# Performance work log

Hardware: AMD Instinct MI355X
Metric: run time of the kernel (lower is better)

Reference implementation:

```python
import math
import jax, jax.numpy as jnp
import numpy as np

N, D = 16384, 1024


def setup_inputs() -> dict:
    key = jax.random.key(0)
    k1, k2 = jax.random.split(key)
    return {
        "image_embeddings_aligned": jax.random.normal(k1, (N, D), dtype=jnp.float32),
        "text_embeddings_aligned": jax.random.normal(k2, (N, D), dtype=jnp.float32),
        "logit_scale": jnp.asarray(math.log(20.0), dtype=jnp.float32),  # stored as log(init)
        "logit_bias": jnp.asarray(-10.0, dtype=jnp.float32),
    }


def _l2_normalize(x, eps=1e-12):
    # matches F.normalize(p=2, dim=-1)
    n = jnp.linalg.norm(x, axis=-1, keepdims=True)
    return x / jnp.maximum(n, eps)


def reference(image_embeddings_aligned, text_embeddings_aligned, logit_scale, logit_bias):
    img = _l2_normalize(image_embeddings_aligned)
    txt = _l2_normalize(text_embeddings_aligned)
    # [N, N] pairwise logits
    logits = jnp.exp(logit_scale) * jnp.einsum("nd,md->nm", img, txt) + logit_bias
    n = logits.shape[0]
    labels = 2.0 * jnp.eye(n, dtype=logits.dtype) - 1.0  # +1 on diagonal, -1 off
    loss_matrix = jax.nn.log_sigmoid(labels * logits)
    siglip_loss = -jnp.mean(loss_matrix)  # total_loss (structure_lambda == 0)
    return siglip_loss
```

## Files before the change

### kernel.cpp

```cpp
#include <hip/hip_runtime.h>

#define NROWS 16384
#define DIM   1024
#define QSCALE 32.0f
#define E8M0S  0x7A7A7A7Au

typedef int    v4i    __attribute__((ext_vector_type(4)));
typedef int    v8i    __attribute__((ext_vector_type(8)));
typedef float  f32x16 __attribute__((ext_vector_type(16)));

__device__ __forceinline__ void glds16(const void* g, void* l) {
    __builtin_amdgcn_global_load_lds(
        (const __attribute__((address_space(1))) void*)g,
        (__attribute__((address_space(3))) void*)l,
        16, 0, 0);
}

__device__ __forceinline__ float fexp2(float x) {
#if __has_builtin(__builtin_amdgcn_exp2f)
    return __builtin_amdgcn_exp2f(x);
#else
    return exp2f(x);
#endif
}
__device__ __forceinline__ float flog2(float x) {
#if __has_builtin(__builtin_amdgcn_logf)
    return __builtin_amdgcn_logf(x);
#else
    return log2f(x);
#endif
}

__device__ __forceinline__ unsigned fp4_nib(float y) {
    unsigned s = (__float_as_uint(y) >> 31) << 3;
    float a = fminf(fabsf(y), 6.0f);
    unsigned c = (unsigned)(a >= 0.25f) + (unsigned)(a >= 0.75f) +
                 (unsigned)(a >= 1.25f) + (unsigned)(a >= 1.75f) +
                 (unsigned)(a >= 2.5f)  + (unsigned)(a >= 3.5f)  +
                 (unsigned)(a >= 5.0f);
    return c | s;
}

__global__ __launch_bounds__(256) void norm_fused(
    const float* __restrict__ img,
    const float* __restrict__ txt,
    unsigned char* __restrict__ imgQ,
    unsigned char* __restrict__ txtQ,
    const float* __restrict__ lscale,
    const float* __restrict__ lbias,
    float* __restrict__ diagPart) {
    const int t    = threadIdx.x;
    const int lane = t & 63;
    const int wave = t >> 6;
    const int gw   = blockIdx.x * 4 + wave;
    const float sc   = __expf(lscale[0]);
    const float bias = lbias[0];

    for (int row = gw; row < NROWS; row += 8192) {
        const float4* pi = (const float4*)(img + (size_t)row * DIM);
        const float4* pt = (const float4*)(txt + (size_t)row * DIM);
        float4 vi[4], vt[4];
        float ssi = 0.0f, sst = 0.0f, dot = 0.0f;
        #pragma unroll
        for (int j = 0; j < 4; ++j) {
            vi[j] = pi[lane + 64 * j];
            vt[j] = pt[lane + 64 * j];
            ssi += vi[j].x*vi[j].x + vi[j].y*vi[j].y + vi[j].z*vi[j].z + vi[j].w*vi[j].w;
            sst += vt[j].x*vt[j].x + vt[j].y*vt[j].y + vt[j].z*vt[j].z + vt[j].w*vt[j].w;
            dot += vi[j].x*vt[j].x + vi[j].y*vt[j].y + vi[j].z*vt[j].z + vi[j].w*vt[j].w;
        }
        #pragma unroll
        for (int off = 1; off < 64; off <<= 1) {
            ssi += __shfl_xor(ssi, off, 64);
            sst += __shfl_xor(sst, off, 64);
            dot += __shfl_xor(dot, off, 64);
        }
        const float ii = 1.0f / fmaxf(sqrtf(ssi), 1e-12f);
        const float it = 1.0f / fmaxf(sqrtf(sst), 1e-12f);
        if (lane == 0) diagPart[row] = -fmaf(sc, dot * ii * it, bias);

        const float qi = ii * QSCALE, qt = it * QSCALE;
        ushort* oi = (ushort*)(imgQ + (size_t)row * 512);
        ushort* ot = (ushort*)(txtQ + (size_t)row * 512);
        #pragma unroll
        for (int j = 0; j < 4; ++j) {
            unsigned p = fp4_nib(vi[j].x * qi)        | (fp4_nib(vi[j].y * qi) << 4) |
                         (fp4_nib(vi[j].z * qi) << 8) | (fp4_nib(vi[j].w * qi) << 12);
            unsigned q = fp4_nib(vt[j].x * qt)        | (fp4_nib(vt[j].y * qt) << 4) |
                         (fp4_nib(vt[j].z * qt) << 8) | (fp4_nib(vt[j].w * qt) << 12);
            oi[lane + 64 * j] = (ushort)p;
            ot[lane + 64 * j] = (ushort)q;
        }
    }
}

__global__ __launch_bounds__(512, 2) void siglip_gemm(
    const unsigned char* __restrict__ A,
    const unsigned char* __restrict__ B,
    const float* __restrict__ lscale,
    const float* __restrict__ lbias,
    float* __restrict__ gemmPart)
{
    __shared__ unsigned char sA[2][256 * 128];
    __shared__ unsigned char sB[2][256 * 128];
    __shared__ float wred[8];

    const int t    = threadIdx.x;
    const int lane = t & 63;
    const int wave = t >> 6;
    const int wr   = wave >> 2;
    const int wc   = wave & 3;
    const int r31  = lane & 31;
    const int h    = lane >> 5;
    const int xr   = (r31 & 7) ^ ((r31 >> 4) & 1);

    const int b    = blockIdx.x;
    const int xcd  = b & 7;
    const int lb   = b >> 3;
    const int bcol = xcd * 8 + (lb & 7);
    const int brow = lb >> 3;

    const size_t aBase = (size_t)brow * 256;
    const size_t bBase = (size_t)bcol * 256;

    const int srow = lane >> 3;
    const int c0   = (lane & 7) ^ srow;
    const int d01  = (c0 & 1) ? -16 : 16;

    const unsigned char* aP = A + (size_t)(aBase + wave * 32 + srow) * 512 + c0 * 16;
    const unsigned char* bP = B + (size_t)(bBase + wave * 32 + srow) * 512 + c0 * 16;

    int rbA[4], rbB[2];
    #pragma unroll
    for (int i = 0; i < 4; ++i) rbA[i] = (wr * 128 + i * 32 + r31) * 128;
    #pragma unroll
    for (int i = 0; i < 2; ++i) rbB[i] = (wc * 64 + i * 32 + r31) * 128;

    f32x16 acc[4][2] = {};

    {
        char* la = ((char*)sA[0]) + wave * 4096;
        char* lb_ = ((char*)sB[0]) + wave * 4096;
        #pragma unroll
        for (int j = 0; j < 4; ++j) {
            const int tog = ((j >> 1) & 1) ? d01 : 0;
            glds16(aP + j * 8 * 512 + tog, la + j * 1024);
            glds16(bP + j * 8 * 512 + tog, lb_ + j * 1024);
        }
    }

    #pragma unroll
    for (int k = 0; k < 4; ++k) {
        const int cur = k & 1;

        if (k < 3) {
            const unsigned char* aN = aP + (k + 1) * 128;
            const unsigned char* bN = bP + (k + 1) * 128;
            char* la = ((char*)sA[cur ^ 1]) + wave * 4096;
            char* lb_ = ((char*)sB[cur ^ 1]) + wave * 4096;
            #pragma unroll
            for (int j = 0; j < 4; ++j) {
                const int tog = ((j >> 1) & 1) ? d01 : 0;
                glds16(aN + j * 8 * 512 + tog, la + j * 1024);
                glds16(bN + j * 8 * 512 + tog, lb_ + j * 1024);
            }
            asm volatile("s_waitcnt vmcnt(8)" ::: "memory");
        } else {
            asm volatile("s_waitcnt vmcnt(0)" ::: "memory");
        }
        __builtin_amdgcn_s_barrier();

        #pragma unroll
        for (int ks = 0; ks < 4; ++ks) {
            const int s = ((ks * 2 + h) ^ xr) * 16;
            v4i av[4], bv[2];
            #pragma unroll
            for (int i = 0; i < 4; ++i)
                av[i] = *(const v4i*)(sA[cur] + rbA[i] + s);
            #pragma unroll
            for (int n = 0; n < 2; ++n)
                bv[n] = *(const v4i*)(sB[cur] + rbB[n] + s);

            __builtin_amdgcn_s_barrier();
            asm volatile("s_waitcnt lgkmcnt(0)" ::: "memory");
            __builtin_amdgcn_sched_barrier(0);
            __builtin_amdgcn_s_setprio(1);
            #pragma unroll
            for (int mi = 0; mi < 4; ++mi) {
                v8i a8 = __builtin_shufflevector(av[mi], av[mi],
                                                 0, 1, 2, 3, -1, -1, -1, -1);
                #pragma unroll
                for (int ni = 0; ni < 2; ++ni) {
                    v8i b8 = __builtin_shufflevector(bv[ni], bv[ni],
                                                     0, 1, 2, 3, -1, -1, -1, -1);
                    acc[mi][ni] = __builtin_amdgcn_mfma_scale_f32_32x32x64_f8f6f4(
                        a8, b8, acc[mi][ni],
                        4, 4,
                        0, (int)E8M0S,
                        0, (int)E8M0S);
                }
            }
            __builtin_amdgcn_s_setprio(0);
            __builtin_amdgcn_s_barrier();
        }
    }

    const float l2e   = 1.44269504088896341f;
    const float scale = __expf(lscale[0]);
    const float aCo   = scale * l2e;
    const float bCo   = lbias[0] * l2e;
    float local = 0.0f;
    #pragma unroll
    for (int mi = 0; mi < 4; ++mi)
        #pragma unroll
        for (int ni = 0; ni < 2; ++ni)
            #pragma unroll
            for (int r = 0; r < 16; r += 4) {
                float e0 = fexp2(fmaf(aCo, acc[mi][ni][r + 0], bCo));
                float e1 = fexp2(fmaf(aCo, acc[mi][ni][r + 1], bCo));
                float e2 = fexp2(fmaf(aCo, acc[mi][ni][r + 2], bCo));
                float e3 = fexp2(fmaf(aCo, acc[mi][ni][r + 3], bCo));
                float p  = ((1.0f + e0) * (1.0f + e1)) *
                           ((1.0f + e2) * (1.0f + e3));
                local += flog2(p);
            }

    #pragma unroll
    for (int off = 32; off > 0; off >>= 1) local += __shfl_down(local, off, 64);
    if (lane == 0) wred[wave] = local;
    __syncthreads();
    if (t == 0) {
        float tot = 0.0f;
        #pragma unroll
        for (int i = 0; i < 8; ++i) tot += wred[i];
        gemmPart[blockIdx.x] = tot * 0.69314718055994531f;
    }
}

__global__ __launch_bounds__(1024) void finalize_kernel(
    const float* __restrict__ parts, float* __restrict__ out) {
    __shared__ float wr[16];
    const int t    = threadIdx.x;
    const int lane = t & 63;
    const int wave = t >> 6;
    const float4* p4 = (const float4*)parts;
    float s = 0.0f;
    for (int i = t; i < 5120; i += 1024) {
        float4 v = p4[i];
        s += v.x + v.y + v.z + v.w;
    }
    #pragma unroll
    for (int off = 32; off > 0; off >>= 1) s += __shfl_down(s, off, 64);
    if (lane == 0) wr[wave] = s;
    __syncthreads();
    if (t == 0) {
        float tot = 0.0f;
        #pragma unroll
        for (int i = 0; i < 16; ++i) tot += wr[i];
        out[0] = tot / 268435456.0f;
    }
}

extern "C" void kernel_launch(void* const* d_in, const int* in_sizes, int n_in,
                              void* d_out, int out_size, void* d_ws, size_t ws_size,
                              hipStream_t stream) {
    const float* img    = (const float*)d_in[0];
    const float* txt    = (const float*)d_in[1];
    const float* lscale = (const float*)d_in[2];
    const float* lbias  = (const float*)d_in[3];
    float* out = (float*)d_out;

    char* ws = (char*)d_ws;
    unsigned char* imgQ = (unsigned char*)ws;
    unsigned char* txtQ = (unsigned char*)(ws + (size_t)NROWS * 512);
    float* parts   = (float*)(ws + (size_t)2 * NROWS * 512);
    float* diagPart = parts;
    float* gemmPart = parts + NROWS;

    norm_fused<<<2048, 256, 0, stream>>>(img, txt, imgQ, txtQ, lscale, lbias, diagPart);
    siglip_gemm<<<dim3((NROWS / 256) * (NROWS / 256)), 512, 0, stream>>>(
        imgQ, txtQ, lscale, lbias, gemmPart);
    finalize_kernel<<<1, 1024, 0, stream>>>(parts, out);
}
```

Measured before the change: 329.8 us.

## Software-pipeline LDS fragment loads and drop per-substep barriers in MFMA loop

Restructures the inner K loop so the LDS fragments for the next sub-step are loaded into a second register set while the current sub-step's MFMAs run, waiting on lgkmcnt(6) instead of draining all LDS reads. The two workgroup barriers per sub-step are removed. Global-to-LDS prefetch now starts after a full vmcnt(0) wait and barrier at the top of each K step rather than a partial wait. This is meant to hide LDS latency and cut synchronization, at the cost of more registers and less overlap of the global prefetch with the wait.

```diff
diff --git a/kernel.cpp b/kernel.cpp
--- a/kernel.cpp
+++ b/kernel.cpp
@@ -153,6 +153,10 @@
     for (int k = 0; k < 4; ++k) {
         const int cur = k & 1;
 
+        asm volatile("s_waitcnt vmcnt(0)" ::: "memory");
+        __builtin_amdgcn_sched_barrier(0);
+        __builtin_amdgcn_s_barrier();
+
         if (k < 3) {
             const unsigned char* aN = aP + (k + 1) * 128;
             const unsigned char* bN = bP + (k + 1) * 128;
@@ -164,44 +168,57 @@
                 glds16(aN + j * 8 * 512 + tog, la + j * 1024);
                 glds16(bN + j * 8 * 512 + tog, lb_ + j * 1024);
             }
-            asm volatile("s_waitcnt vmcnt(8)" ::: "memory");
-        } else {
-            asm volatile("s_waitcnt vmcnt(0)" ::: "memory");
-        }
-        __builtin_amdgcn_s_barrier();
+        }
+
+        v4i pa[2][4], pb[2][2];
+        {
+            const int s0 = (h ^ xr) * 16;
+            #pragma unroll
+            for (int i = 0; i < 4; ++i)
+                pa[0][i] = *(const v4i*)(sA[cur] + rbA[i] + s0);
+            #pragma unroll
+            for (int n = 0; n < 2; ++n)
+                pb[0][n] = *(const v4i*)(sB[cur] + rbB[n] + s0);
+        }
 
         #pragma unroll
         for (int ks = 0; ks < 4; ++ks) {
-            const int s = ((ks * 2 + h) ^ xr) * 16;
-            v4i av[4], bv[2];
+            const int pc = ks & 1, pn = pc ^ 1;
+            if (ks < 3) {
+                const int s1 = (((ks + 1) * 2 + h) ^ xr) * 16;
+                #pragma unroll
+                for (int i = 0; i < 4; ++i)
+                    pa[pn][i] = *(const v4i*)(sA[cur] + rbA[i] + s1);
+                #pragma unroll
+                for (int n = 0; n < 2; ++n)
+                    pb[pn][n] = *(const v4i*)(sB[cur] + rbB[n] + s1);
+                asm volatile("s_waitcnt lgkmcnt(6)" ::: "memory");
+            } else {
+                asm volatile("s_waitcnt lgkmcnt(0)" ::: "memory");
+            }
+            __builtin_amdgcn_sched_barrier(0);
+
+            v8i a8[4], b8[2];
             #pragma unroll
             for (int i = 0; i < 4; ++i)
-                av[i] = *(const v4i*)(sA[cur] + rbA[i] + s);
+                a8[i] = __builtin_shufflevector(pa[pc][i], pa[pc][i],
+                                                0, 1, 2, 3, -1, -1, -1, -1);
             #pragma unroll
             for (int n = 0; n < 2; ++n)
-                bv[n] = *(const v4i*)(sB[cur] + rbB[n] + s);
-
-            __builtin_amdgcn_s_barrier();
-            asm volatile("s_waitcnt lgkmcnt(0)" ::: "memory");
-            __builtin_amdgcn_sched_barrier(0);
+                b8[n] = __builtin_shufflevector(pb[pc][n], pb[pc][n],
+                                                0, 1, 2, 3, -1, -1, -1, -1);
+
             __builtin_amdgcn_s_setprio(1);
             #pragma unroll
-            for (int mi = 0; mi < 4; ++mi) {
-                v8i a8 = __builtin_shufflevector(av[mi], av[mi],
-                                                 0, 1, 2, 3, -1, -1, -1, -1);
+            for (int mi = 0; mi < 4; ++mi)
                 #pragma unroll
-                for (int ni = 0; ni < 2; ++ni) {
-                    v8i b8 = __builtin_shufflevector(bv[ni], bv[ni],
-                                                     0, 1, 2, 3, -1, -1, -1, -1);
+                for (int ni = 0; ni < 2; ++ni)
                     acc[mi][ni] = __builtin_amdgcn_mfma_scale_f32_32x32x64_f8f6f4(
-                        a8, b8, acc[mi][ni],
+                        a8[mi], b8[ni], acc[mi][ni],
                         4, 4,
                         0, (int)E8M0S,
                         0, (int)E8M0S);
-                }
-            }
             __builtin_amdgcn_s_setprio(0);
-            __builtin_amdgcn_s_barrier();
         }
     }
 
```

Measured after the change: 312.7 us. -5.2%, faster.

## Interleave next-tile global-to-LDS loads across MFMA sub-steps

Applied to the files above, without the earlier changes.

Moves the prefetch of the next K tile from a single burst at the top of each iteration into the first three of the four MFMA sub-steps, issuing two or three global_load_lds ops per sub-step. The wait on those loads now happens at the end of the last sub-step, and the separate per-iteration barrier is removed. The aim is to spread memory issue across MFMA work and shorten the exposed wait before each barrier. The trade-off is a full vmcnt(0) wait at the end of each iteration instead of a partial vmcnt(8) wait, so load latency can become exposed if the sub-steps finish early.

```diff
diff --git a/kernel.cpp b/kernel.cpp
--- a/kernel.cpp
+++ b/kernel.cpp
@@ -147,32 +147,22 @@
             glds16(aP + j * 8 * 512 + tog, la + j * 1024);
             glds16(bP + j * 8 * 512 + tog, lb_ + j * 1024);
         }
-    }
+        asm volatile("s_waitcnt vmcnt(0)" ::: "memory");
+    }
+    __builtin_amdgcn_s_barrier();
 
     #pragma unroll
     for (int k = 0; k < 4; ++k) {
         const int cur = k & 1;
-
-        if (k < 3) {
-            const unsigned char* aN = aP + (k + 1) * 128;
-            const unsigned char* bN = bP + (k + 1) * 128;
-            char* la = ((char*)sA[cur ^ 1]) + wave * 4096;
-            char* lb_ = ((char*)sB[cur ^ 1]) + wave * 4096;
-            #pragma unroll
-            for (int j = 0; j < 4; ++j) {
-                const int tog = ((j >> 1) & 1) ? d01 : 0;
-                glds16(aN + j * 8 * 512 + tog, la + j * 1024);
-                glds16(bN + j * 8 * 512 + tog, lb_ + j * 1024);
-            }
-            asm volatile("s_waitcnt vmcnt(8)" ::: "memory");
-        } else {
-            asm volatile("s_waitcnt vmcnt(0)" ::: "memory");
-        }
-        __builtin_amdgcn_s_barrier();
-
-        #pragma unroll
-        for (int ks = 0; ks < 4; ++ks) {
-            const int s = ((ks * 2 + h) ^ xr) * 16;
+        const bool stage = (k < 3);
+        const unsigned char* aN = aP + (k + 1) * 128;
+        const unsigned char* bN = bP + (k + 1) * 128;
+        char* laN = ((char*)sA[cur ^ 1]) + wave * 4096;
+        char* lbN = ((char*)sB[cur ^ 1]) + wave * 4096;
+
+        #pragma unroll
+        for (int p = 0; p < 4; ++p) {
+            const int s = ((p * 2 + h) ^ xr) * 16;
             v4i av[4], bv[2];
             #pragma unroll
             for (int i = 0; i < 4; ++i)
@@ -180,27 +170,52 @@
             #pragma unroll
             for (int n = 0; n < 2; ++n)
                 bv[n] = *(const v4i*)(sB[cur] + rbB[n] + s);
+
+            if (stage) {
+                if (p == 0) {
+                    glds16(aN,                laN);
+                    glds16(aN + 4096,         laN + 1024);
+                    glds16(aN + 8192  + d01,  laN + 2048);
+                } else if (p == 1) {
+                    glds16(aN + 12288 + d01,  laN + 3072);
+                    glds16(bN,                lbN);
+                    glds16(bN + 4096,         lbN + 1024);
+                } else if (p == 2) {
+                    glds16(bN + 8192  + d01,  lbN + 2048);
+                    glds16(bN + 12288 + d01,  lbN + 3072);
+                }
+            }
 
             __builtin_amdgcn_s_barrier();
             asm volatile("s_waitcnt lgkmcnt(0)" ::: "memory");
             __builtin_amdgcn_sched_barrier(0);
+
+            v8i a8[4], b8[2];
+            #pragma unroll
+            for (int i = 0; i < 4; ++i)
+                a8[i] = __builtin_shufflevector(av[i], av[i],
+                                                0, 1, 2, 3, -1, -1, -1, -1);
+            #pragma unroll
+            for (int n = 0; n < 2; ++n)
+                b8[n] = __builtin_shufflevector(bv[n], bv[n],
+                                                0, 1, 2, 3, -1, -1, -1, -1);
+
             __builtin_amdgcn_s_setprio(1);
             #pragma unroll
-            for (int mi = 0; mi < 4; ++mi) {
-                v8i a8 = __builtin_shufflevector(av[mi], av[mi],
-                                                 0, 1, 2, 3, -1, -1, -1, -1);
+            for (int mi = 0; mi < 4; ++mi)
                 #pragma unroll
-                for (int ni = 0; ni < 2; ++ni) {
-                    v8i b8 = __builtin_shufflevector(bv[ni], bv[ni],
-                                                     0, 1, 2, 3, -1, -1, -1, -1);
+                for (int ni = 0; ni < 2; ++ni)
                     acc[mi][ni] = __builtin_amdgcn_mfma_scale_f32_32x32x64_f8f6f4(
-                        a8, b8, acc[mi][ni],
+                        a8[mi], b8[ni], acc[mi][ni],
                         4, 4,
                         0, (int)E8M0S,
                         0, (int)E8M0S);
-                }
+            __builtin_amdgcn_s_setprio(0);
+
+            if (p == 3 && stage) {
+                asm volatile("s_waitcnt vmcnt(0)" ::: "memory");
+                __builtin_amdgcn_sched_barrier(0);
             }
-            __builtin_amdgcn_s_setprio(0);
             __builtin_amdgcn_s_barrier();
         }
     }
```

Result: faster. 322.3 us (-2.3%).
